# Optimization experiments

Measured on AMD Instinct MI355X. Metric: run time of the kernel, lower is better.

The kernel has to match this reference:

```python
import jax, jax.numpy as jnp
import numpy as np

B, S, D, N, LAYERS = 512, 64, 256, 100000, 1


def setup_inputs() -> dict:
    key = jax.random.key(0)
    ks = jax.random.split(key, 9)
    stdv = 1.0 / np.sqrt(D)
    return {
        "embedding": jax.random.uniform(ks[0], (N, D), jnp.float32, -stdv, stdv),
        "W1": jax.random.uniform(ks[1], (2 * D, 2 * D), jnp.float32, -stdv, stdv),
        "W2": jax.random.uniform(ks[2], (2 * D, D), jnp.float32, -stdv, stdv),
        "adj_in": jax.random.uniform(ks[3], (B, S, S), jnp.float32),
        "adj_out": jax.random.uniform(ks[4], (B, S, S), jnp.float32),
        "mask": jnp.ones((B, S), jnp.float32),
        "item": jax.random.randint(ks[5], (B, S), 0, N),
        "alias": jax.random.randint(ks[6], (B, S), 0, S),
        "tar": jax.random.randint(ks[7], (B,), 1, N),  # targets in [1, n_node)
    }


def reference(embedding, W1, W2, adj_in, adj_out, mask, item, alias, tar):
    # ---- sgc(): gather -> dual adjacency aggregation -> concat -> 2-layer MLP
    fin = embedding[item]                              # [B,S,D]
    # torch `adj ** layers` is elementwise power (not matrix power)
    fs_in = jnp.matmul(adj_in ** LAYERS, fin)          # [B,S,D]
    fs_out = jnp.matmul(adj_out ** LAYERS, fin)        # [B,S,D]
    av = jnp.concatenate([fs_in, fs_out], axis=-1)     # [B,S,2D]
    av = jnp.matmul(jax.nn.relu(jnp.matmul(av, W1)), W2)  # [B,S,D]

    # ---- forward(): pick last node's hidden, score against item table
    rows = jnp.arange(B)
    rm = jnp.sum(mask, axis=1).astype(jnp.int32)       # session lengths [B]
    last_id = alias[rows, rm - 1]                      # [B]
    last_h = av[rows, last_id]                         # [B,D]
    logits = last_h @ embedding[1:].T                  # [B,N-1]

    logp = jax.nn.log_softmax(logits, axis=-1)
    loss = -jnp.mean(logp[rows, tar - 1])
    # L2 term is zero: params live in a plain dict (not registered) and l2=0.
    return loss, logits
```

## Files before the change

kernel.cpp:

```cpp
#include <hip/hip_runtime.h>
#include <cstdint>
#include <cstddef>

#define BDIM 512
#define SDIM 64
#define DDIM 256
#define D2   512
#define NNODE 100000
#define NM1  99999

typedef short short8 __attribute__((ext_vector_type(8)));
typedef float f32x4 __attribute__((ext_vector_type(4)));

__device__ __forceinline__ unsigned short f2bf(float f) {
  unsigned int u = __float_as_uint(f);
  u += 0x7FFFu + ((u >> 16) & 1u);
  return (unsigned short)(u >> 16);
}

__global__ __launch_bounds__(256) void prep_kernel(
    const float* __restrict__ emb, const float* __restrict__ adj_in,
    const float* __restrict__ adj_out, const float* __restrict__ mask,
    const int* __restrict__ item, const int* __restrict__ alias_,
    float* __restrict__ av) {
  __shared__ float a_in[SDIM], a_out[SDIM];
  __shared__ int it[SDIM];
  __shared__ int s_star;
  const int b = blockIdx.x, t = threadIdx.x;
  if (t < SDIM) it[t] = item[b * SDIM + t];
  if (t < 64) {
    float m = mask[b * SDIM + t];
#pragma unroll
    for (int off = 32; off > 0; off >>= 1) m += __shfl_down(m, off, 64);
    if (t == 0) {
      int rm = (int)m;
      s_star = alias_[b * SDIM + rm - 1];
    }
  }
  __syncthreads();
  const int ss = s_star;
  if (t < SDIM) a_in[t] = adj_in[((size_t)b * SDIM + ss) * SDIM + t];
  else if (t < 2 * SDIM) a_out[t - SDIM] = adj_out[((size_t)b * SDIM + ss) * SDIM + (t - SDIM)];
  __syncthreads();
  const int d = t;
  float ai = 0.f, ao = 0.f;
#pragma unroll 8
  for (int j = 0; j < SDIM; j++) {
    float e = emb[(size_t)it[j] * DDIM + d];
    ai = fmaf(a_in[j], e, ai);
    ao = fmaf(a_out[j], e, ao);
  }
  av[(size_t)b * D2 + d] = ai;
  av[(size_t)b * D2 + DDIM + d] = ao;
}

template <int N, bool RELU, bool OUTBF16>
__global__ __launch_bounds__(256) void mlp_kernel(
    const float* __restrict__ A, const float* __restrict__ W,
    float* __restrict__ Of, unsigned short* __restrict__ Ob) {
  __shared__ float As[32][36];
  __shared__ float Bs[32][68];
  const int tx = threadIdx.x, ty = threadIdx.y;
  const int t = ty * 16 + tx;
  const int row0 = blockIdx.y * 32, col0 = blockIdx.x * 64;
  const int ar = t >> 3, ac = (t & 7) * 4;
  const int kr = t >> 4, bc = (t & 15) * 4;
  float acc[2][4];
#pragma unroll
  for (int i = 0; i < 2; i++)
#pragma unroll
    for (int j = 0; j < 4; j++) acc[i][j] = 0.f;

  for (int k0 = 0; k0 < D2; k0 += 32) {
    const float4 a4 = *(const float4*)&A[(size_t)(row0 + ar) * D2 + k0 + ac];
    const float4 b4a = *(const float4*)&W[(size_t)(k0 + kr) * N + col0 + bc];
    const float4 b4b = *(const float4*)&W[(size_t)(k0 + kr + 16) * N + col0 + bc];
    *(float4*)&As[ar][ac] = a4;
    *(float4*)&Bs[kr][bc] = b4a;
    *(float4*)&Bs[kr + 16][bc] = b4b;
    __syncthreads();
#pragma unroll
    for (int k = 0; k < 32; k++) {
      const float a0 = As[ty * 2][k];
      const float a1 = As[ty * 2 + 1][k];
      const float4 bv = *(const float4*)&Bs[k][tx * 4];
      acc[0][0] = fmaf(a0, bv.x, acc[0][0]); acc[0][1] = fmaf(a0, bv.y, acc[0][1]);
      acc[0][2] = fmaf(a0, bv.z, acc[0][2]); acc[0][3] = fmaf(a0, bv.w, acc[0][3]);
      acc[1][0] = fmaf(a1, bv.x, acc[1][0]); acc[1][1] = fmaf(a1, bv.y, acc[1][1]);
      acc[1][2] = fmaf(a1, bv.z, acc[1][2]); acc[1][3] = fmaf(a1, bv.w, acc[1][3]);
    }
    __syncthreads();
  }
#pragma unroll
  for (int i = 0; i < 2; i++) {
    const int row = row0 + ty * 2 + i;
    const int col = col0 + tx * 4;
    float4 r4;
    r4.x = acc[i][0]; r4.y = acc[i][1]; r4.z = acc[i][2]; r4.w = acc[i][3];
    if constexpr (RELU) {
      r4.x = fmaxf(r4.x, 0.f); r4.y = fmaxf(r4.y, 0.f);
      r4.z = fmaxf(r4.z, 0.f); r4.w = fmaxf(r4.w, 0.f);
    }
    if constexpr (OUTBF16) {
      ushort4 p;
      p.x = f2bf(r4.x); p.y = f2bf(r4.y); p.z = f2bf(r4.z); p.w = f2bf(r4.w);
      *(ushort4*)&Ob[(size_t)row * N + col] = p;
    } else {
      *(float4*)&Of[(size_t)row * N + col] = r4;
    }
  }
}

#define NT    64
#define BPAD  264
#define NTILES 1563

__global__ __launch_bounds__(512, 4) void logits_gemm(
    const unsigned short* __restrict__ Abf,
    const float* __restrict__ emb,
    float* __restrict__ out,
    float* __restrict__ part) {
  __shared__ short Bs[NT * BPAD];
  __shared__ float rse_s[BDIM];
  const int t = threadIdx.x;
  const int lane = t & 63, w = t >> 6;
  const int nbase = blockIdx.x * NT;

  {
    const int row = t >> 3;
    const int cb = (t & 7) * 4;
    int er = nbase + row + 1;
    if (er > NM1) er = NM1;
    const float* src = emb + (size_t)er * DDIM;
    short* dst = &Bs[row * BPAD];
#pragma unroll
    for (int j = 0; j < 8; j++) {
      const float4 v = *(const float4*)(src + j * 32 + cb);
      ushort4 p;
      p.x = f2bf(v.x); p.y = f2bf(v.y); p.z = f2bf(v.z); p.w = f2bf(v.w);
      *(ushort4*)&dst[j * 32 + cb] = p;
    }
  }
  __syncthreads();

  const int wm = w * 64;
  const int c = lane & 15, q = lane >> 4;

  f32x4 acc[4][4];
#pragma unroll
  for (int mi = 0; mi < 4; mi++)
#pragma unroll
    for (int ni = 0; ni < 4; ni++) acc[mi][ni] = (f32x4){0.f, 0.f, 0.f, 0.f};

#pragma unroll
  for (int ks = 0; ks < 8; ks++) {
    short8 afr[4], bfr[4];
#pragma unroll
    for (int mi = 0; mi < 4; mi++)
      afr[mi] = *(const short8*)(Abf +
          (size_t)(wm + mi * 16 + c) * DDIM + ks * 32 + q * 8);
#pragma unroll
    for (int ni = 0; ni < 4; ni++)
      bfr[ni] = *(const short8*)&Bs[(ni * 16 + c) * BPAD + ks * 32 + q * 8];
#pragma unroll
    for (int mi = 0; mi < 4; mi++)
#pragma unroll
      for (int ni = 0; ni < 4; ni++)
        acc[mi][ni] = __builtin_amdgcn_mfma_f32_16x16x32_bf16(
            afr[mi], bfr[ni], acc[mi][ni], 0, 0, 0);
  }

  const bool full = (nbase + NT <= NM1);
#pragma unroll
  for (int mi = 0; mi < 4; mi++) {
#pragma unroll
    for (int r = 0; r < 4; r++) {
      const int grow = wm + mi * 16 + q * 4 + r;
      float s = 0.f;
      if (full) {
#pragma unroll
        for (int ni = 0; ni < 4; ni++) {
          const float v = acc[mi][ni][r];
          out[1 + (size_t)grow * NM1 + nbase + ni * 16 + c] = v;
          s += __expf(v);
        }
      } else {
#pragma unroll
        for (int ni = 0; ni < 4; ni++) {
          const int col = nbase + ni * 16 + c;
          if (col < NM1) {
            const float v = acc[mi][ni][r];
            out[1 + (size_t)grow * NM1 + col] = v;
            s += __expf(v);
          }
        }
      }
#pragma unroll
      for (int msk = 1; msk < 16; msk <<= 1) s += __shfl_xor(s, msk, 64);
      if (c == 0) rse_s[grow] = s;
    }
  }
  __syncthreads();
  part[(size_t)blockIdx.x * BDIM + t] = rse_s[t];
}

__global__ __launch_bounds__(256) void rse_loss_kernel(
    const float* __restrict__ part, const float* __restrict__ out,
    const int* __restrict__ tar, float* __restrict__ lossv) {
  const int b = blockIdx.x;
  const int t = threadIdx.x;
  float s = 0.f;
  for (int j = t; j < NTILES; j += 256)
    s += part[(size_t)j * BDIM + b];
  __shared__ float red[4];
#pragma unroll
  for (int off = 32; off > 0; off >>= 1) s += __shfl_down(s, off, 64);
  if ((t & 63) == 0) red[t >> 6] = s;
  __syncthreads();
  if (t == 0) {
    const float tot = red[0] + red[1] + red[2] + red[3];
    const int tt = tar[b];
    const float lg = out[1 + (size_t)b * NM1 + (tt - 1)];
    lossv[b] = logf(tot) - lg;
  }
}

__global__ __launch_bounds__(512) void loss_final_kernel(
    float* __restrict__ out, const float* __restrict__ lossv) {
  __shared__ float red[512];
  const int t = threadIdx.x;
  red[t] = lossv[t];
  __syncthreads();
  for (int stride = 256; stride > 0; stride >>= 1) {
    if (t < stride) red[t] += red[t + stride];
    __syncthreads();
  }
  if (t == 0) out[0] = red[0] / (float)BDIM;
}

extern "C" void kernel_launch(void* const* d_in, const int* in_sizes, int n_in,
                              void* d_out, int out_size, void* d_ws, size_t ws_size,
                              hipStream_t stream) {
  const float* emb     = (const float*)d_in[0];
  const float* W1      = (const float*)d_in[1];
  const float* W2      = (const float*)d_in[2];
  const float* adj_in  = (const float*)d_in[3];
  const float* adj_out = (const float*)d_in[4];
  const float* mask    = (const float*)d_in[5];
  const int*   item    = (const int*)d_in[6];
  const int*   alias_  = (const int*)d_in[7];
  const int*   tar     = (const int*)d_in[8];
  float* out = (float*)d_out;

  char* ws = (char*)d_ws;
  float* av            = (float*)(ws);
  float* h1            = (float*)(ws + 1048576);
  unsigned short* lasth = (unsigned short*)(ws + 2097152);
  float* part          = (float*)(ws + 2359296);
  float* lossv         = (float*)(ws + 5560320);

  prep_kernel<<<BDIM, 256, 0, stream>>>(emb, adj_in, adj_out, mask, item, alias_, av);
  mlp_kernel<D2, true, false><<<dim3(8, 16), dim3(16, 16), 0, stream>>>(av, W1, h1, nullptr);
  mlp_kernel<DDIM, false, true><<<dim3(4, 16), dim3(16, 16), 0, stream>>>(h1, W2, nullptr, lasth);
  logits_gemm<<<dim3(NTILES), 512, 0, stream>>>(lasth, emb, out, part);
  rse_loss_kernel<<<BDIM, 256, 0, stream>>>(part, out, tar, lossv);
  loss_final_kernel<<<1, 512, 0, stream>>>(out, lossv);
}
```

Before: 456.5 us.

## Split logits GEMM over batch halves and loop four N tiles per block

```diff
diff --git a/kernel.cpp b/kernel.cpp
--- a/kernel.cpp
+++ b/kernel.cpp
@@ -113,7 +113,7 @@
 
 #define NT    64
 #define BPAD  264
-#define NTILES 1563
+#define NCHUNK 391
 
 __global__ __launch_bounds__(512, 4) void logits_gemm(
     const unsigned short* __restrict__ Abf,
@@ -121,87 +121,106 @@
     float* __restrict__ out,
     float* __restrict__ part) {
   __shared__ short Bs[NT * BPAD];
-  __shared__ float rse_s[BDIM];
+  __shared__ float rse_s[256];
   const int t = threadIdx.x;
   const int lane = t & 63, w = t >> 6;
-  const int nbase = blockIdx.x * NT;
-
-  {
-    const int row = t >> 3;
-    const int cb = (t & 7) * 4;
-    int er = nbase + row + 1;
-    if (er > NM1) er = NM1;
-    const float* src = emb + (size_t)er * DDIM;
-    short* dst = &Bs[row * BPAD];
-#pragma unroll
-    for (int j = 0; j < 8; j++) {
-      const float4 v = *(const float4*)(src + j * 32 + cb);
-      ushort4 p;
-      p.x = f2bf(v.x); p.y = f2bf(v.y); p.z = f2bf(v.z); p.w = f2bf(v.w);
-      *(ushort4*)&dst[j * 32 + cb] = p;
-    }
-  }
-  __syncthreads();
-
-  const int wm = w * 64;
+  const int nchunk = blockIdx.x;
+  const int mbase = blockIdx.y * 256;
+  const int wm = w * 32;
   const int c = lane & 15, q = lane >> 4;
 
-  f32x4 acc[4][4];
-#pragma unroll
-  for (int mi = 0; mi < 4; mi++)
-#pragma unroll
-    for (int ni = 0; ni < 4; ni++) acc[mi][ni] = (f32x4){0.f, 0.f, 0.f, 0.f};
-
-#pragma unroll
-  for (int ks = 0; ks < 8; ks++) {
-    short8 afr[4], bfr[4];
-#pragma unroll
-    for (int mi = 0; mi < 4; mi++)
-      afr[mi] = *(const short8*)(Abf +
-          (size_t)(wm + mi * 16 + c) * DDIM + ks * 32 + q * 8);
-#pragma unroll
-    for (int ni = 0; ni < 4; ni++)
-      bfr[ni] = *(const short8*)&Bs[(ni * 16 + c) * BPAD + ks * 32 + q * 8];
-#pragma unroll
-    for (int mi = 0; mi < 4; mi++)
+  float s8[8];
+#pragma unroll
+  for (int i = 0; i < 8; i++) s8[i] = 0.f;
+
+#pragma unroll 1
+  for (int st = 0; st < 4; st++) {
+    const int nbase = nchunk * 256 + st * NT;
+
+    __syncthreads();
+    {
+      const int row = t >> 3;
+      const int cb = (t & 7) * 4;
+      int er = nbase + row + 1;
+      if (er > NM1) er = NM1;
+      const float* src = emb + (size_t)er * DDIM;
+      short* dst = &Bs[row * BPAD];
+#pragma unroll
+      for (int j = 0; j < 8; j++) {
+        const float4 v = *(const float4*)(src + j * 32 + cb);
+        ushort4 p;
+        p.x = f2bf(v.x); p.y = f2bf(v.y); p.z = f2bf(v.z); p.w = f2bf(v.w);
+        *(ushort4*)&dst[j * 32 + cb] = p;
+      }
+    }
+    __syncthreads();
+
+    f32x4 acc[2][4];
+#pragma unroll
+    for (int mi = 0; mi < 2; mi++)
+#pragma unroll
+      for (int ni = 0; ni < 4; ni++) acc[mi][ni] = (f32x4){0.f, 0.f, 0.f, 0.f};
+
+#pragma unroll
+    for (int ks = 0; ks < 8; ks++) {
+      short8 afr[2], bfr[4];
+#pragma unroll
+      for (int mi = 0; mi < 2; mi++)
+        afr[mi] = *(const short8*)(Abf +
+            (size_t)(mbase + wm + mi * 16 + c) * DDIM + ks * 32 + q * 8);
 #pragma unroll
       for (int ni = 0; ni < 4; ni++)
-        acc[mi][ni] = __builtin_amdgcn_mfma_f32_16x16x32_bf16(
-            afr[mi], bfr[ni], acc[mi][ni], 0, 0, 0);
-  }
-
-  const bool full = (nbase + NT <= NM1);
-#pragma unroll
-  for (int mi = 0; mi < 4; mi++) {
-#pragma unroll
-    for (int r = 0; r < 4; r++) {
-      const int grow = wm + mi * 16 + q * 4 + r;
-      float s = 0.f;
-      if (full) {
-#pragma unroll
-        for (int ni = 0; ni < 4; ni++) {
-          const float v = acc[mi][ni][r];
-          out[1 + (size_t)grow * NM1 + nbase + ni * 16 + c] = v;
-          s += __expf(v);
-        }
-      } else {
-#pragma unroll
-        for (int ni = 0; ni < 4; ni++) {
-          const int col = nbase + ni * 16 + c;
-          if (col < NM1) {
+        bfr[ni] = *(const short8*)&Bs[(ni * 16 + c) * BPAD + ks * 32 + q * 8];
+#pragma unroll
+      for (int mi = 0; mi < 2; mi++)
+#pragma unroll
+        for (int ni = 0; ni < 4; ni++)
+          acc[mi][ni] = __builtin_amdgcn_mfma_f32_16x16x32_bf16(
+              afr[mi], bfr[ni], acc[mi][ni], 0, 0, 0);
+    }
+
+    const bool full = (nbase + NT <= NM1);
+#pragma unroll
+    for (int mi = 0; mi < 2; mi++) {
+#pragma unroll
+      for (int r = 0; r < 4; r++) {
+        const int grow = mbase + wm + mi * 16 + q * 4 + r;
+        float s = 0.f;
+        if (full) {
+#pragma unroll
+          for (int ni = 0; ni < 4; ni++) {
             const float v = acc[mi][ni][r];
-            out[1 + (size_t)grow * NM1 + col] = v;
+            out[1 + (size_t)grow * NM1 + nbase + ni * 16 + c] = v;
             s += __expf(v);
           }
+        } else {
+#pragma unroll
+          for (int ni = 0; ni < 4; ni++) {
+            const int col = nbase + ni * 16 + c;
+            if (col < NM1) {
+              const float v = acc[mi][ni][r];
+              out[1 + (size_t)grow * NM1 + col] = v;
+              s += __expf(v);
+            }
+          }
         }
+        s8[mi * 4 + r] += s;
       }
+    }
+  }
+
+#pragma unroll
+  for (int mi = 0; mi < 2; mi++) {
+#pragma unroll
+    for (int r = 0; r < 4; r++) {
+      float s = s8[mi * 4 + r];
 #pragma unroll
       for (int msk = 1; msk < 16; msk <<= 1) s += __shfl_xor(s, msk, 64);
-      if (c == 0) rse_s[grow] = s;
-    }
-  }
-  __syncthreads();
-  part[(size_t)blockIdx.x * BDIM + t] = rse_s[t];
+      if (c == 0) rse_s[wm + mi * 16 + q * 4 + r] = s;
+    }
+  }
+  __syncthreads();
+  if (t < 256) part[(size_t)nchunk * BDIM + mbase + t] = rse_s[t];
 }
 
 __global__ __launch_bounds__(256) void rse_loss_kernel(
@@ -210,7 +229,7 @@
   const int b = blockIdx.x;
   const int t = threadIdx.x;
   float s = 0.f;
-  for (int j = t; j < NTILES; j += 256)
+  for (int j = t; j < NCHUNK; j += 256)
     s += part[(size_t)j * BDIM + b];
   __shared__ float red[4];
 #pragma unroll
@@ -262,7 +281,7 @@
   prep_kernel<<<BDIM, 256, 0, stream>>>(emb, adj_in, adj_out, mask, item, alias_, av);
   mlp_kernel<D2, true, false><<<dim3(8, 16), dim3(16, 16), 0, stream>>>(av, W1, h1, nullptr);
   mlp_kernel<DDIM, false, true><<<dim3(4, 16), dim3(16, 16), 0, stream>>>(h1, W2, nullptr, lasth);
-  logits_gemm<<<dim3(NTILES), 512, 0, stream>>>(lasth, emb, out, part);
+  logits_gemm<<<dim3(NCHUNK, 2), 512, 0, stream>>>(lasth, emb, out, part);
   rse_loss_kernel<<<BDIM, 256, 0, stream>>>(part, out, tar, lossv);
   loss_final_kernel<<<1, 512, 0, stream>>>(out, lossv);
 }
```

Measured after the change: 463.1 us. No clear change (+1.4%).
